# Optimization experiments

Measured on AMD Instinct MI355X. Metric: run time of the kernel, lower is better.

Reference implementation:

```python
import jax, jax.numpy as jnp
import numpy as np

N, E, DIN, DOUT = 100000, 500000, 256, 1


def setup_inputs() -> dict:
    key = jax.random.key(0)
    k1, k2, k3, k4 = jax.random.split(key, 4)
    x = jax.random.normal(k1, (N, DIN), dtype=jnp.float32)
    edge_label_index = jax.random.randint(k2, (2, E), 0, N, dtype=jnp.int64)
    # nn.Linear default init: U(-1/sqrt(fan_in), 1/sqrt(fan_in)); plain scaled normal is fine for a numeric reference
    W1 = jax.random.normal(k3, (2 * DIN, DIN), dtype=jnp.float32) / np.sqrt(2 * DIN)
    b1 = jnp.zeros((DIN,), dtype=jnp.float32)
    W2 = jax.random.normal(k4, (DIN, DOUT), dtype=jnp.float32) / np.sqrt(DIN)
    b2 = jnp.zeros((DOUT,), dtype=jnp.float32)
    return {"x": x, "edge_label_index": edge_label_index, "W1": W1, "b1": b1, "W2": W2, "b2": b2}


def reference(x, edge_label_index, W1, b1, W2, b2):
    x_i = x[edge_label_index[0]]            # [E, DIN] gather src
    x_j = x[edge_label_index[1]]            # [E, DIN] gather dst
    h = jnp.concatenate([x_i, x_j], axis=-1)  # [E, 2*DIN]
    h = jax.nn.relu(h @ W1 + b1)            # [E, DIN]
    return h @ W2 + b2                      # [E, DOUT]
```

## Files before the change

kernel.cpp:

```cpp
#include <hip/hip_runtime.h>
#include <hip/hip_bf16.h>


typedef short short8 __attribute__((ext_vector_type(8)));
typedef float f32x4 __attribute__((ext_vector_type(4)));

#define DINC 256
#define NOUTC 512

__device__ inline unsigned short f2bf(float f) {
  union { float f; unsigned u; } c; c.f = f;
  unsigned u = c.u;
  return (unsigned short)((u + 0x7FFFu + ((u >> 16) & 1u)) >> 16);
}
__device__ inline float bf2f(unsigned short h) {
  union { unsigned u; float f; } c; c.u = ((unsigned)h) << 16;
  return c.f;
}
__device__ inline unsigned short fbf(float f) {
  union { __hip_bfloat16 h; unsigned short u; } c;
  c.h = __float2bfloat16(f);
  return c.u;
}

__global__ void w1t_kernel(const float* __restrict__ W1, unsigned short* __restrict__ W1t) {
  int t = blockIdx.x * 256 + threadIdx.x;
  int lane = t & 63, nf = (t >> 6) & 7, kt = (t >> 9) & 7, bn = t >> 12;
  int col = bn * 128 + nf * 16 + (lane & 15);
  int k0 = kt * 32 + (lane >> 4) * 8;
  int off = (col >= 256) ? 256 : 0;
  int cs = col & 255;
  short8 v;
#pragma unroll
  for (int j = 0; j < 8; ++j)
    v[j] = (short)f2bf(W1[(size_t)(k0 + j + off) * DINC + cs]);
  *(short8*)(W1t + (size_t)t * 8) = v;
}

__global__ __launch_bounds__(256) void cvt_kernel(const float* __restrict__ x,
                                                  unsigned short* __restrict__ xbf,
                                                  int Nn) {
  int g = blockIdx.x * 256 + threadIdx.x;
  int lane = g & 63, kt = (g >> 6) & 7, c = g >> 9;
  int row = c * 16 + (lane & 15);
  if (row >= Nn) row = Nn - 1;
  int k0 = kt * 32 + (lane >> 4) * 8;
  const float4* xp = (const float4*)(x + (size_t)row * DINC + k0);
  float4 f0 = xp[0], f1 = xp[1];
  short8 v;
  v[0] = (short)fbf(f0.x); v[1] = (short)fbf(f0.y);
  v[2] = (short)fbf(f0.z); v[3] = (short)fbf(f0.w);
  v[4] = (short)fbf(f1.x); v[5] = (short)fbf(f1.y);
  v[6] = (short)fbf(f1.z); v[7] = (short)fbf(f1.w);
  *(short8*)(xbf + (size_t)g * 8) = v;
}

__global__ __launch_bounds__(256, 1) void uv_gemm(const unsigned short* __restrict__ xbf,
                                                  const unsigned short* __restrict__ W1t,
                                                  unsigned short* __restrict__ uv,
                                                  int Nn) {
  __shared__ unsigned short Bs[128 * DINC];

  int L = (blockIdx.x & 7) * (gridDim.x >> 3) + (blockIdx.x >> 3);
  int bn = L & 3, rank = L >> 2;

  int tid = threadIdx.x, lane = tid & 63, w = tid >> 6;
  int lr = lane & 15, kg = lane >> 4;

  {
    const char* bsrc = (const char*)W1t + (size_t)bn * 65536;
#pragma unroll
    for (int i = 0; i < 16; ++i) {
      int o = i * 4096 + w * 1024;
      __builtin_amdgcn_global_load_lds(
          (const __attribute__((address_space(1))) void*)(bsrc + o + lane * 16),
          (__attribute__((address_space(3))) void*)((char*)Bs + o), 16, 0, 0);
    }
  }
  __syncthreads();

  int nch = (Nn + 15) >> 4;
  int stream = rank * 4 + w;
  const int S = 512;
  const char* xb = (const char*)xbf;

#define LOADH(BUF, C)                                                          \
  {                                                                            \
    const char* p_ = xb + (size_t)(C) * 8192 + lane * 16;                      \
    _Pragma("unroll")                                                          \
    for (int kt = 0; kt < 8; ++kt)                                             \
      BUF[kt] = *(const short8*)(p_ + kt * 1024);                              \
  }

#define CS(BUF, C)                                                             \
  {                                                                            \
    f32x4 acc[8] = {};                                                         \
    _Pragma("unroll")                                                          \
    for (int kt = 0; kt < 8; ++kt) {                                           \
      _Pragma("unroll")                                                        \
      for (int nf = 0; nf < 8; ++nf) {                                         \
        short8 bf_ = *(const short8*)((char*)Bs + ((kt * 8 + nf) * 64 + lane) * 16); \
        acc[nf] = __builtin_amdgcn_mfma_f32_16x16x32_bf16(bf_, BUF[kt],        \
                                                          acc[nf], 0, 0, 0);   \
      }                                                                        \
    }                                                                          \
    int row_ = (C) * 16 + lr;                                                  \
    if (row_ < Nn) {                                                           \
      unsigned short* orow_ = uv + (size_t)row_ * NOUTC + bn * 128 + kg * 4;   \
      _Pragma("unroll")                                                        \
      for (int nf = 0; nf < 8; ++nf) {                                         \
        ushort4 pk;                                                            \
        pk.x = fbf(acc[nf][0]); pk.y = fbf(acc[nf][1]);                        \
        pk.z = fbf(acc[nf][2]); pk.w = fbf(acc[nf][3]);                        \
        *(ushort4*)(orow_ + nf * 16) = pk;                                     \
      }                                                                        \
    }                                                                          \
  }

  short8 A0[8], A1[8];
  int c = stream;
  if (c < nch) {
    LOADH(A0, c);
    for (;;) {
      int c1 = c + S;
      if (c1 < nch) {
        LOADH(A1, c1);
        CS(A0, c);
        int c2 = c1 + S;
        if (c2 < nch) {
          LOADH(A0, c2);
          CS(A1, c1);
          c = c2;
        } else { CS(A1, c1); break; }
      } else { CS(A0, c); break; }
    }
  }
#undef LOADH
#undef CS
}

__global__ __launch_bounds__(256) void edge_kernel(const int* __restrict__ eliW,
                                                   const unsigned short* __restrict__ uv,
                                                   const float* __restrict__ b1,
                                                   const float* __restrict__ W2,
                                                   const float* __restrict__ b2,
                                                   float* __restrict__ out, int E) {
  int tid = threadIdx.x;
  int ql = tid & 15;
  bool is64 = ((eliW[1] | eliW[3] | eliW[5] | eliW[7] | eliW[9] | eliW[11]) == 0);
  int shift = is64 ? 1 : 0;

  float bl[16], wl[16];
  *(float4*)(bl + 0)  = *(const float4*)(b1 + ql * 8);
  *(float4*)(bl + 4)  = *(const float4*)(b1 + ql * 8 + 4);
  *(float4*)(bl + 8)  = *(const float4*)(b1 + 128 + ql * 8);
  *(float4*)(bl + 12) = *(const float4*)(b1 + 128 + ql * 8 + 4);
  *(float4*)(wl + 0)  = *(const float4*)(W2 + ql * 8);
  *(float4*)(wl + 4)  = *(const float4*)(W2 + ql * 8 + 4);
  *(float4*)(wl + 8)  = *(const float4*)(W2 + 128 + ql * 8);
  *(float4*)(wl + 12) = *(const float4*)(W2 + 128 + ql * 8 + 4);
  float bias2 = b2[0];

  int qid = (blockIdx.x * blockDim.x + tid) >> 4;
  int nq = (gridDim.x * blockDim.x) >> 4;

  for (int e = qid; e < E; e += nq) {
    int src = eliW[((size_t)e) << shift];
    int dst = eliW[((size_t)(E + e)) << shift];
    const unsigned short* up = uv + (size_t)src * NOUTC;
    const unsigned short* vp = uv + (size_t)dst * NOUTC + DINC;
    short8 uu[2], vv[2];
    uu[0] = *(const short8*)(up + ql * 8);
    uu[1] = *(const short8*)(up + 128 + ql * 8);
    vv[0] = *(const short8*)(vp + ql * 8);
    vv[1] = *(const short8*)(vp + 128 + ql * 8);
    float s = 0.f;
#pragma unroll
    for (int g = 0; g < 2; ++g)
#pragma unroll
      for (int j = 0; j < 8; ++j) {
        float h = bf2f((unsigned short)uu[g][j]) + bf2f((unsigned short)vv[g][j]) + bl[g * 8 + j];
        s += fmaxf(h, 0.f) * wl[g * 8 + j];
      }
#pragma unroll
    for (int off = 8; off; off >>= 1) s += __shfl_xor(s, off, 64);
    if (ql == 0) out[e] = s + bias2;
  }
}

extern "C" void kernel_launch(void* const* d_in, const int* in_sizes, int n_in,
                              void* d_out, int out_size, void* d_ws, size_t ws_size,
                              hipStream_t stream) {
  const float* x   = (const float*)d_in[0];
  const int*   eli = (const int*)d_in[1];
  const float* W1  = (const float*)d_in[2];
  const float* b1  = (const float*)d_in[3];
  const float* W2  = (const float*)d_in[4];
  const float* b2  = (const float*)d_in[5];
  float* out = (float*)d_out;

  int Nn = in_sizes[0] / DINC;
  int E  = in_sizes[1] / 2;
  int nch = (Nn + 15) >> 4;

  unsigned short* W1t = (unsigned short*)d_ws;
  unsigned short* uv  = W1t + (size_t)NOUTC * DINC;
  unsigned short* xbf = uv + (size_t)Nn * NOUTC;

  w1t_kernel<<<64, 256, 0, stream>>>(W1, W1t);
  cvt_kernel<<<nch * 2, 256, 0, stream>>>(x, xbf, Nn);

  uv_gemm<<<512, 256, 0, stream>>>(xbf, W1t, uv, Nn);

  edge_kernel<<<2048, 256, 0, stream>>>(eli, uv, b1, W2, b2, out, E);
}
```

Before: 153.1 us.

## Fuse bf16 conversion into GEMM loads and unroll edge kernel by two

Removes the separate fp32-to-bf16 conversion kernel and intermediate buffer, having the GEMM load fp32 rows of x directly and convert in registers before MFMA. The edge kernel now processes two edges per iteration to issue more independent gathers. The trade-off is that each of the four column blocks reads fp32 x, doubling per-pass bytes versus bf16, and larger register buffers.

```diff
diff --git a/kernel.cpp b/kernel.cpp
--- a/kernel.cpp
+++ b/kernel.cpp
@@ -37,25 +37,7 @@
   *(short8*)(W1t + (size_t)t * 8) = v;
 }
 
-__global__ __launch_bounds__(256) void cvt_kernel(const float* __restrict__ x,
-                                                  unsigned short* __restrict__ xbf,
-                                                  int Nn) {
-  int g = blockIdx.x * 256 + threadIdx.x;
-  int lane = g & 63, kt = (g >> 6) & 7, c = g >> 9;
-  int row = c * 16 + (lane & 15);
-  if (row >= Nn) row = Nn - 1;
-  int k0 = kt * 32 + (lane >> 4) * 8;
-  const float4* xp = (const float4*)(x + (size_t)row * DINC + k0);
-  float4 f0 = xp[0], f1 = xp[1];
-  short8 v;
-  v[0] = (short)fbf(f0.x); v[1] = (short)fbf(f0.y);
-  v[2] = (short)fbf(f0.z); v[3] = (short)fbf(f0.w);
-  v[4] = (short)fbf(f1.x); v[5] = (short)fbf(f1.y);
-  v[6] = (short)fbf(f1.z); v[7] = (short)fbf(f1.w);
-  *(short8*)(xbf + (size_t)g * 8) = v;
-}
-
-__global__ __launch_bounds__(256, 1) void uv_gemm(const unsigned short* __restrict__ xbf,
+__global__ __launch_bounds__(256, 1) void uv_gemm(const float* __restrict__ x,
                                                   const unsigned short* __restrict__ W1t,
                                                   unsigned short* __restrict__ uv,
                                                   int Nn) {
@@ -82,14 +64,17 @@
   int nch = (Nn + 15) >> 4;
   int stream = rank * 4 + w;
   const int S = 512;
-  const char* xb = (const char*)xbf;
 
 #define LOADH(BUF, C)                                                          \
   {                                                                            \
-    const char* p_ = xb + (size_t)(C) * 8192 + lane * 16;                      \
-    _Pragma("unroll")                                                          \
-    for (int kt = 0; kt < 8; ++kt)                                             \
-      BUF[kt] = *(const short8*)(p_ + kt * 1024);                              \
+    int row_ = (C) * 16 + lr;                                                  \
+    if (row_ >= Nn) row_ = Nn - 1;                                             \
+    const float4* xp_ = (const float4*)(x + (size_t)row_ * DINC + kg * 8);     \
+    _Pragma("unroll")                                                          \
+    for (int kt = 0; kt < 8; ++kt) {                                           \
+      BUF[2 * kt]     = xp_[kt * 8];                                           \
+      BUF[2 * kt + 1] = xp_[kt * 8 + 1];                                       \
+    }                                                                          \
   }
 
 #define CS(BUF, C)                                                             \
@@ -97,10 +82,16 @@
     f32x4 acc[8] = {};                                                         \
     _Pragma("unroll")                                                          \
     for (int kt = 0; kt < 8; ++kt) {                                           \
+      float4 f0 = BUF[2 * kt], f1 = BUF[2 * kt + 1];                           \
+      short8 a;                                                                \
+      a[0] = (short)fbf(f0.x); a[1] = (short)fbf(f0.y);                        \
+      a[2] = (short)fbf(f0.z); a[3] = (short)fbf(f0.w);                        \
+      a[4] = (short)fbf(f1.x); a[5] = (short)fbf(f1.y);                        \
+      a[6] = (short)fbf(f1.z); a[7] = (short)fbf(f1.w);                        \
       _Pragma("unroll")                                                        \
       for (int nf = 0; nf < 8; ++nf) {                                         \
         short8 bf_ = *(const short8*)((char*)Bs + ((kt * 8 + nf) * 64 + lane) * 16); \
-        acc[nf] = __builtin_amdgcn_mfma_f32_16x16x32_bf16(bf_, BUF[kt],        \
+        acc[nf] = __builtin_amdgcn_mfma_f32_16x16x32_bf16(bf_, a,              \
                                                           acc[nf], 0, 0, 0);   \
       }                                                                        \
     }                                                                          \
@@ -117,7 +108,7 @@
     }                                                                          \
   }
 
-  short8 A0[8], A1[8];
+  float4 A0[16], A1[16];
   int c = stream;
   if (c < nch) {
     LOADH(A0, c);
@@ -164,28 +155,55 @@
   int qid = (blockIdx.x * blockDim.x + tid) >> 4;
   int nq = (gridDim.x * blockDim.x) >> 4;
 
-  for (int e = qid; e < E; e += nq) {
-    int src = eliW[((size_t)e) << shift];
-    int dst = eliW[((size_t)(E + e)) << shift];
-    const unsigned short* up = uv + (size_t)src * NOUTC;
-    const unsigned short* vp = uv + (size_t)dst * NOUTC + DINC;
-    short8 uu[2], vv[2];
-    uu[0] = *(const short8*)(up + ql * 8);
-    uu[1] = *(const short8*)(up + 128 + ql * 8);
-    vv[0] = *(const short8*)(vp + ql * 8);
-    vv[1] = *(const short8*)(vp + 128 + ql * 8);
-    float s = 0.f;
-#pragma unroll
-    for (int g = 0; g < 2; ++g)
-#pragma unroll
-      for (int j = 0; j < 8; ++j) {
-        float h = bf2f((unsigned short)uu[g][j]) + bf2f((unsigned short)vv[g][j]) + bl[g * 8 + j];
-        s += fmaxf(h, 0.f) * wl[g * 8 + j];
-      }
-#pragma unroll
-    for (int off = 8; off; off >>= 1) s += __shfl_xor(s, off, 64);
-    if (ql == 0) out[e] = s + bias2;
-  }
+#define DOT(UU, VV, SREG)                                                      \
+  {                                                                            \
+    float s_ = 0.f;                                                            \
+    _Pragma("unroll")                                                          \
+    for (int g = 0; g < 2; ++g)                                                \
+      _Pragma("unroll")                                                        \
+      for (int j = 0; j < 8; ++j) {                                            \
+        float h = bf2f((unsigned short)UU[g][j]) +                             \
+                  bf2f((unsigned short)VV[g][j]) + bl[g * 8 + j];              \
+        s_ += fmaxf(h, 0.f) * wl[g * 8 + j];                                   \
+      }                                                                        \
+    _Pragma("unroll")                                                          \
+    for (int off = 8; off; off >>= 1) s_ += __shfl_xor(s_, off, 64);           \
+    SREG = s_;                                                                 \
+  }
+
+  for (int e = qid; e < E; e += 2 * nq) {
+    int e1 = e + nq;
+    bool has1 = e1 < E;
+    int e1c = has1 ? e1 : e;
+    int src0 = eliW[((size_t)e) << shift];
+    int dst0 = eliW[((size_t)(E + e)) << shift];
+    int src1 = eliW[((size_t)e1c) << shift];
+    int dst1 = eliW[((size_t)(E + e1c)) << shift];
+
+    const unsigned short* up0 = uv + (size_t)src0 * NOUTC;
+    const unsigned short* vp0 = uv + (size_t)dst0 * NOUTC + DINC;
+    const unsigned short* up1 = uv + (size_t)src1 * NOUTC;
+    const unsigned short* vp1 = uv + (size_t)dst1 * NOUTC + DINC;
+
+    short8 uu0[2], vv0[2], uu1[2], vv1[2];
+    uu0[0] = *(const short8*)(up0 + ql * 8);
+    uu0[1] = *(const short8*)(up0 + 128 + ql * 8);
+    vv0[0] = *(const short8*)(vp0 + ql * 8);
+    vv0[1] = *(const short8*)(vp0 + 128 + ql * 8);
+    uu1[0] = *(const short8*)(up1 + ql * 8);
+    uu1[1] = *(const short8*)(up1 + 128 + ql * 8);
+    vv1[0] = *(const short8*)(vp1 + ql * 8);
+    vv1[1] = *(const short8*)(vp1 + 128 + ql * 8);
+
+    float s0, s1;
+    DOT(uu0, vv0, s0);
+    DOT(uu1, vv1, s1);
+    if (ql == 0) {
+      out[e] = s0 + bias2;
+      if (has1) out[e1] = s1 + bias2;
+    }
+  }
+#undef DOT
 }
 
 extern "C" void kernel_launch(void* const* d_in, const int* in_sizes, int n_in,
@@ -201,16 +219,13 @@
 
   int Nn = in_sizes[0] / DINC;
   int E  = in_sizes[1] / 2;
-  int nch = (Nn + 15) >> 4;
 
   unsigned short* W1t = (unsigned short*)d_ws;
   unsigned short* uv  = W1t + (size_t)NOUTC * DINC;
-  unsigned short* xbf = uv + (size_t)Nn * NOUTC;
 
   w1t_kernel<<<64, 256, 0, stream>>>(W1, W1t);
-  cvt_kernel<<<nch * 2, 256, 0, stream>>>(x, xbf, Nn);
-
-  uv_gemm<<<512, 256, 0, stream>>>(xbf, W1t, uv, Nn);
+
+  uv_gemm<<<512, 256, 0, stream>>>(x, W1t, uv, Nn);
 
   edge_kernel<<<2048, 256, 0, stream>>>(eli, uv, b1, W2, b2, out, E);
 }
```

Measured after the change: 161.0 us. +5.2%, slower.
